# Optimization experiments

Measured on AMD Instinct MI355X. Metric: run time of the kernel, lower is better.

## Reference

```python
import jax, jax.numpy as jnp
import numpy as np

C = 256
RED = 8
DQK = C // RED  # 32


def setup_inputs() -> dict:
    key = jax.random.key(0)
    ks = jax.random.split(key, 8)
    B, H, W = 8, 64, 64
    x = jax.random.normal(ks[0], (B, C, H, W), dtype=jnp.float32)
    # 1x1 conv weights stored as [out, in]; biases [out]
    Wq = jax.random.normal(ks[1], (DQK, C), dtype=jnp.float32) * 0.02
    bq = jax.random.normal(ks[2], (DQK,), dtype=jnp.float32) * 0.02
    Wk = jax.random.normal(ks[3], (DQK, C), dtype=jnp.float32) * 0.02
    bk = jax.random.normal(ks[4], (DQK,), dtype=jnp.float32) * 0.02
    Wv = jax.random.normal(ks[5], (C, C), dtype=jnp.float32) * 0.02
    bv = jax.random.normal(ks[6], (C,), dtype=jnp.float32) * 0.02
    gamma = jax.random.normal(ks[7], (1,), dtype=jnp.float32) * 0.1
    return {"x": x, "Wq": Wq, "bq": bq, "Wk": Wk, "bk": bk, "Wv": Wv, "bv": bv, "gamma": gamma}


def reference(x, Wq, bq, Wk, bk, Wv, bv, gamma):
    B, Cc, H, W = x.shape
    N = H * W
    xf = x.reshape(B, Cc, N)                       # (B, C, N)
    # 1x1 convs == per-pixel dense projections
    q = jnp.einsum('dc,bcn->bdn', Wq, xf) + bq[None, :, None]   # (B, d, N)
    k = jnp.einsum('dc,bcn->bdn', Wk, xf) + bk[None, :, None]   # (B, d, N)
    v = jnp.einsum('ec,bcn->ben', Wv, xf) + bv[None, :, None]   # (B, C, N)
    # energy[b,i,j] = q[b,:,i] . k[b,:,j]; softmax over j (no scaling, SAGAN-style)
    energy = jnp.einsum('bdi,bdj->bij', q, k)      # (B, N, N)
    attn = jax.nn.softmax(energy, axis=-1)
    # out[b,c,i] = sum_j v[b,c,j] * attn[b,i,j]
    out = jnp.einsum('bcj,bij->bci', v, attn)      # (B, C, N)
    out = out.reshape(B, Cc, H, W)
    return gamma[0] * out + x
```

## Files before the change

kernel.cpp:

```cpp
#include <hip/hip_runtime.h>

#define NB 8
#define CCH 256
#define DQK 32
#define NPIX 4096

typedef __attribute__((ext_vector_type(8))) short short8;
typedef __attribute__((ext_vector_type(4))) float f32x4;
typedef __attribute__((ext_vector_type(4))) unsigned short ushort4v;

static __device__ __forceinline__ unsigned short f2bf(float f) {
  unsigned int u = __builtin_bit_cast(unsigned int, f);
  u += 0x7FFFu + ((u >> 16) & 1u);
  return (unsigned short)(u >> 16);
}
static __device__ __forceinline__ unsigned int pack2bf(float a, float b) {
  return (unsigned int)f2bf(a) | ((unsigned int)f2bf(b) << 16);
}

__global__ __launch_bounds__(256) void wconv_kernel(
    const float* __restrict__ Wq, const float* __restrict__ Wk,
    const float* __restrict__ Wv, unsigned short* __restrict__ Wbf) {
  const int e = (blockIdx.x * 256 + threadIdx.x) * 4;
  const int m = e >> 8, c = e & 255;
  const float* src;
  if (m < 32) src = Wq + (size_t)m * CCH;
  else if (m < 64) src = Wk + (size_t)(m - 32) * CCH;
  else src = Wv + (size_t)(m - 64) * CCH;
  const float4 v = *(const float4*)(src + c);
  ushort4v o;
  o[0] = f2bf(v.x); o[1] = f2bf(v.y); o[2] = f2bf(v.z); o[3] = f2bf(v.w);
  *(ushort4v*)(Wbf + e) = o;
}

__global__ __launch_bounds__(256) void proj_kernel(
    const float* __restrict__ x, const unsigned short* __restrict__ Wbf,
    const float* __restrict__ bq, const float* __restrict__ bk,
    const float* __restrict__ bv,
    unsigned short* __restrict__ Qb, unsigned short* __restrict__ Kb,
    unsigned short* __restrict__ Vb) {
  __shared__ unsigned short xs[32 * 256];
  const int t = threadIdx.x;
  const int b = blockIdx.x & 7;
  const int i0 = (blockIdx.x >> 3) * 32;
  const float* xb = x + (size_t)b * CCH * NPIX + i0;
  {
    const int ii = (t & 7) * 4;
    const int cb = t >> 3;
    const int sw8 = ((ii >> 2) & 7) << 3;
#pragma unroll
    for (int rep = 0; rep < 8; ++rep) {
      const int c = cb + 32 * rep;
      const float4 v = *(const float4*)(xb + (size_t)c * NPIX + ii);
      const float vv[4] = {v.x, v.y, v.z, v.w};
#pragma unroll
      for (int d = 0; d < 4; ++d) {
        const int cc = (c ^ sw8) ^ ((d & 1) << 4);
        xs[(ii + d) * 256 + cc] = f2bf(vv[d]);
      }
    }
  }
  __syncthreads();
  const int w = t >> 6, l = t & 63;
  const int lc = l & 15, lg = l >> 4;
  const int m0w = 80 * w;
  f32x4 acc[5][2];
#pragma unroll
  for (int mt = 0; mt < 5; ++mt)
#pragma unroll
    for (int nt = 0; nt < 2; ++nt) acc[mt][nt] = (f32x4){0.f, 0.f, 0.f, 0.f};

#pragma unroll
  for (int kk = 0; kk < 8; ++kk) {
    short8 af[5];
#pragma unroll
    for (int mt = 0; mt < 5; ++mt)
      af[mt] = *(const short8*)(Wbf + (size_t)(m0w + mt * 16 + lc) * CCH + kk * 32 + lg * 8);
#pragma unroll
    for (int nt = 0; nt < 2; ++nt) {
      const int i = nt * 16 + lc;
      const int s = (4 * nt + (lc >> 2)) & 7;
      const int cc = ((kk * 32 + lg * 8) ^ (s << 3)) ^ ((lc & 1) << 4);
      const short8 bfv = *(const short8*)&xs[i * 256 + cc];
#pragma unroll
      for (int mt = 0; mt < 5; ++mt)
        acc[mt][nt] = __builtin_amdgcn_mfma_f32_16x16x32_bf16(af[mt], bfv, acc[mt][nt], 0, 0, 0);
    }
  }
#pragma unroll
  for (int mt = 0; mt < 5; ++mt) {
    const int mbase = m0w + mt * 16;
    const int mrow = mbase + 4 * lg;
    if (mbase < 64) {
      const float* bias = (mbase < 32) ? (bq + mrow) : (bk + (mrow - 32));
      unsigned short* dst = (mbase < 32) ? (Qb + (size_t)b * NPIX * DQK + mrow)
                                         : (Kb + (size_t)b * NPIX * DQK + (mrow - 32));
      const float b0 = bias[0], b1 = bias[1], b2 = bias[2], b3 = bias[3];
#pragma unroll
      for (int nt = 0; nt < 2; ++nt) {
        const int i = i0 + nt * 16 + lc;
        ushort4v o;
        o[0] = f2bf(acc[mt][nt][0] + b0);
        o[1] = f2bf(acc[mt][nt][1] + b1);
        o[2] = f2bf(acc[mt][nt][2] + b2);
        o[3] = f2bf(acc[mt][nt][3] + b3);
        *(ushort4v*)(dst + (size_t)i * DQK) = o;
      }
    } else {
      const int vrow = mbase - 64 + 4 * lg;
#pragma unroll
      for (int jj = 0; jj < 4; ++jj) {
        const float bias = bv[vrow + jj];
        unsigned short* vdst = Vb + ((size_t)b * CCH + vrow + jj) * NPIX + i0;
#pragma unroll
        for (int nt = 0; nt < 2; ++nt)
          vdst[nt * 16 + lc] = f2bf(acc[mt][nt][jj] + bias);
      }
    }
  }
}

union AttnSmem {
  unsigned short p[2][64 * 64];
  float tsc[4][16 * 68];
};

__global__ __launch_bounds__(256, 2) void attn_kernel(
    const unsigned short* __restrict__ Qb,
    const unsigned short* __restrict__ Kb,
    const unsigned short* __restrict__ Vb,
    const float* __restrict__ x,
    const float* __restrict__ gammap,
    float* __restrict__ out) {
  __shared__ AttnSmem sm;
  __shared__ float l_lds[64];
  const int t = threadIdx.x;
  const int w = t >> 6, l = t & 63;
  const int lc = l & 15, lg = l >> 4;
  const int b = blockIdx.x & 7;
  const int q0 = (blockIdx.x >> 3) * 64;

  const unsigned short* Kl = Kb + (size_t)b * NPIX * DQK + (size_t)lc * DQK + lg * 8;
  const unsigned short* Vl = Vb + ((size_t)b * CCH + 64 * w + lc) * NPIX + lg * 8;
  const short8 qa = *(const short8*)(Qb + (size_t)b * NPIX * DQK +
                                     (size_t)(q0 + 16 * w + lc) * DQK + lg * 8);
  const f32x4 zero4 = {0.f, 0.f, 0.f, 0.f};
  const int pwb = (16 * w + lc) * 128;
  const int psw = (lc & 7) << 3;

  f32x4 acc[4][4];
#pragma unroll
  for (int mt = 0; mt < 4; ++mt)
#pragma unroll
    for (int ct = 0; ct < 4; ++ct) acc[mt][ct] = (f32x4){0.f, 0.f, 0.f, 0.f};
  float psum = 0.f;

  short8 vfA[8], vfB[8], kfA[4], kfB[4];

#pragma unroll
  for (int kt = 0; kt < 4; ++kt)
    kfA[kt] = *(const short8*)(Kl + (size_t)(kt * 16) * DQK);
#pragma unroll
  for (int kt = 0; kt < 4; ++kt) {
    const f32x4 s = __builtin_amdgcn_mfma_f32_16x16x32_bf16(kfA[kt], qa, zero4, 0, 0, 0);
    const float p0 = __expf(s[0]), p1 = __expf(s[1]);
    const float p2 = __expf(s[2]), p3 = __expf(s[3]);
    psum += (p0 + p1) + (p2 + p3);
    uint2 wv; wv.x = pack2bf(p0, p1); wv.y = pack2bf(p2, p3);
    *(uint2*)((char*)sm.p[0] + pwb + (((16 * kt + 4 * lg) ^ psw) << 1)) = wv;
  }
#pragma unroll
  for (int ct = 0; ct < 4; ++ct) {
    vfA[ct] = *(const short8*)(Vl + (size_t)(16 * ct) * NPIX);
    vfA[4 + ct] = *(const short8*)(Vl + (size_t)(16 * ct) * NPIX + 32);
  }
#pragma unroll
  for (int kt = 0; kt < 4; ++kt)
    kfB[kt] = *(const short8*)(Kl + (size_t)(64 + kt * 16) * DQK);
  __syncthreads();

#define ATTN_ITER(T, BUF, VF, KF_CUR, VF_NXT, KF_NXT)                               \
  {                                                                                 \
    const int t_ = (T);                                                             \
    if (t_ < 63) {                                                                  \
      const size_t kb2 = (size_t)(t_ + 1) * 64;                                     \
      _Pragma("unroll") for (int ct = 0; ct < 4; ++ct) {                            \
        VF_NXT[ct] = *(const short8*)(Vl + (size_t)(16 * ct) * NPIX + kb2);         \
        VF_NXT[4 + ct] = *(const short8*)(Vl + (size_t)(16 * ct) * NPIX + kb2 + 32);\
      }                                                                             \
      if (t_ < 62) {                                                                \
        const size_t kk2 = (size_t)(t_ + 2) * 64;                                   \
        _Pragma("unroll") for (int kt = 0; kt < 4; ++kt)                            \
          KF_NXT[kt] = *(const short8*)(Kl + (kk2 + kt * 16) * DQK);                \
      }                                                                             \
    }                                                                               \
    unsigned short* pb_ = sm.p[BUF];                                                \
    unsigned short* pb2_ = sm.p[(BUF) ^ 1];                                         \
    _Pragma("unroll") for (int ks2 = 0; ks2 < 2; ++ks2) {                           \
      short8 pa[4];                                                                 \
      _Pragma("unroll") for (int mt = 0; mt < 4; ++mt)                              \
        pa[mt] = *(const short8*)((const char*)pb_ + (16 * mt + lc) * 128 +         \
                                  (((32 * ks2 + 8 * lg) ^ psw) << 1));              \
      _Pragma("unroll") for (int ct = 0; ct < 4; ++ct)                              \
        _Pragma("unroll") for (int mt = 0; mt < 4; ++mt)                            \
          acc[mt][ct] = __builtin_amdgcn_mfma_f32_16x16x32_bf16(                    \
              pa[mt], VF[ks2 * 4 + ct], acc[mt][ct], 0, 0, 0);                      \
    }                                                                               \
    if (t_ < 63) {                                                                  \
      _Pragma("unroll") for (int kt = 0; kt < 4; ++kt) {                            \
        const f32x4 s = __builtin_amdgcn_mfma_f32_16x16x32_bf16(                    \
            KF_CUR[kt], qa, zero4, 0, 0, 0);                                        \
        const float p0 = __expf(s[0]), p1 = __expf(s[1]);                           \
        const float p2 = __expf(s[2]), p3 = __expf(s[3]);                           \
        psum += (p0 + p1) + (p2 + p3);                                              \
        uint2 wv; wv.x = pack2bf(p0, p1); wv.y = pack2bf(p2, p3);                   \
        *(uint2*)((char*)pb2_ + pwb + (((16 * kt + 4 * lg) ^ psw) << 1)) = wv;      \
      }                                                                             \
    }                                                                               \
    __syncthreads();                                                                \
  }

  for (int ks = 0; ks < 64; ks += 2) {
    ATTN_ITER(ks, 0, vfA, kfB, vfB, kfA);
    ATTN_ITER(ks + 1, 1, vfB, kfA, vfA, kfB);
  }
#undef ATTN_ITER

  {
    float v = psum;
    v += __shfl_xor(v, 16);
    v += __shfl_xor(v, 32);
    if (l < 16) l_lds[16 * w + lc] = v;
  }
  __syncthreads();

  const float g = gammap[0];
  float linv4[4][4];
#pragma unroll
  for (int mt = 0; mt < 4; ++mt)
#pragma unroll
    for (int jj = 0; jj < 4; ++jj)
      linv4[mt][jj] = 1.0f / l_lds[16 * mt + 4 * lg + jj];

  float* tw = sm.tsc[w];
  const float* xbp = x + (size_t)b * CCH * NPIX;
  float* ob = out + (size_t)b * CCH * NPIX;
#pragma unroll
  for (int ct = 0; ct < 4; ++ct) {
#pragma unroll
    for (int mt = 0; mt < 4; ++mt) {
      f32x4 o;
#pragma unroll
      for (int jj = 0; jj < 4; ++jj) o[jj] = g * acc[mt][ct][jj] * linv4[mt][jj];
      *(f32x4*)(tw + lc * 68 + 16 * mt + 4 * lg) = o;
    }
#pragma unroll
    for (int r = 0; r < 4; ++r) {
      const int crow = 4 * r + lg;
      const f32x4 o = *(const f32x4*)(tw + crow * 68 + lc * 4);
      const size_t idx = (size_t)(64 * w + 16 * ct + crow) * NPIX + (size_t)(q0 + lc * 4);
      const float4 xv = *(const float4*)(xbp + idx);
      float4 ov;
      ov.x = o[0] + xv.x; ov.y = o[1] + xv.y; ov.z = o[2] + xv.z; ov.w = o[3] + xv.w;
      *(float4*)(ob + idx) = ov;
    }
  }
}

extern "C" void kernel_launch(void* const* d_in, const int* in_sizes, int n_in,
                              void* d_out, int out_size, void* d_ws, size_t ws_size,
                              hipStream_t stream) {
  (void)in_sizes; (void)n_in; (void)out_size; (void)ws_size;
  const float* x     = (const float*)d_in[0];
  const float* Wq    = (const float*)d_in[1];
  const float* bq    = (const float*)d_in[2];
  const float* Wk    = (const float*)d_in[3];
  const float* bk    = (const float*)d_in[4];
  const float* Wv    = (const float*)d_in[5];
  const float* bv    = (const float*)d_in[6];
  const float* gamma = (const float*)d_in[7];

  unsigned short* Wbf = (unsigned short*)d_ws;
  unsigned short* Qb  = Wbf + 320 * CCH;
  unsigned short* Kb  = Qb + (size_t)NB * NPIX * DQK;
  unsigned short* Vb  = Kb + (size_t)NB * NPIX * DQK;

  wconv_kernel<<<80, 256, 0, stream>>>(Wq, Wk, Wv, Wbf);
  proj_kernel<<<1024, 256, 0, stream>>>(x, Wbf, bq, bk, bv, Qb, Kb, Vb);
  attn_kernel<<<512, 256, 0, stream>>>(Qb, Kb, Vb, x, gamma, (float*)d_out);
}
```

Before: 272.9 us.

## Use exp2 with prescaled Q, packed bf16 convert, and reschedule attention MFMAs

Q is now prescaled by log2(e) in the projection kernel, so the attention kernel can call exp2 directly instead of expf. The manual bf16 rounding is replaced by the hardware v_cvt_pk_bf16_f32 instruction. The QK score MFMAs are issued before the PV MFMAs so their latency overlaps. Both P fragment halves are loaded up front and the PV block runs under raised s_setprio. __syncthreads is replaced by an explicit lgkmcnt wait plus s_barrier, and gamma is folded into the reciprocal of the row sum. Rounding in the packed convert may differ slightly from the manual version, and holding extra fragments live raises register pressure.

```diff
diff --git a/kernel.cpp b/kernel.cpp
--- a/kernel.cpp
+++ b/kernel.cpp
@@ -14,8 +14,10 @@
   u += 0x7FFFu + ((u >> 16) & 1u);
   return (unsigned short)(u >> 16);
 }
-static __device__ __forceinline__ unsigned int pack2bf(float a, float b) {
-  return (unsigned int)f2bf(a) | ((unsigned int)f2bf(b) << 16);
+static __device__ __forceinline__ unsigned int cvt_pk_bf16(float a, float b) {
+  unsigned int r;
+  asm("v_cvt_pk_bf16_f32 %0, %1, %2" : "=v"(r) : "v"(a), "v"(b));
+  return r;
 }
 
 __global__ __launch_bounds__(256) void wconv_kernel(
@@ -92,18 +94,20 @@
     const int mbase = m0w + mt * 16;
     const int mrow = mbase + 4 * lg;
     if (mbase < 64) {
-      const float* bias = (mbase < 32) ? (bq + mrow) : (bk + (mrow - 32));
-      unsigned short* dst = (mbase < 32) ? (Qb + (size_t)b * NPIX * DQK + mrow)
-                                         : (Kb + (size_t)b * NPIX * DQK + (mrow - 32));
+      const bool isQ = (mbase < 32);
+      const float scale = isQ ? 1.44269504f : 1.0f;
+      const float* bias = isQ ? (bq + mrow) : (bk + (mrow - 32));
+      unsigned short* dst = isQ ? (Qb + (size_t)b * NPIX * DQK + mrow)
+                                : (Kb + (size_t)b * NPIX * DQK + (mrow - 32));
       const float b0 = bias[0], b1 = bias[1], b2 = bias[2], b3 = bias[3];
 #pragma unroll
       for (int nt = 0; nt < 2; ++nt) {
         const int i = i0 + nt * 16 + lc;
         ushort4v o;
-        o[0] = f2bf(acc[mt][nt][0] + b0);
-        o[1] = f2bf(acc[mt][nt][1] + b1);
-        o[2] = f2bf(acc[mt][nt][2] + b2);
-        o[3] = f2bf(acc[mt][nt][3] + b3);
+        o[0] = f2bf((acc[mt][nt][0] + b0) * scale);
+        o[1] = f2bf((acc[mt][nt][1] + b1) * scale);
+        o[2] = f2bf((acc[mt][nt][2] + b2) * scale);
+        o[3] = f2bf((acc[mt][nt][3] + b3) * scale);
         *(ushort4v*)(dst + (size_t)i * DQK) = o;
       }
     } else {
@@ -163,10 +167,10 @@
 #pragma unroll
   for (int kt = 0; kt < 4; ++kt) {
     const f32x4 s = __builtin_amdgcn_mfma_f32_16x16x32_bf16(kfA[kt], qa, zero4, 0, 0, 0);
-    const float p0 = __expf(s[0]), p1 = __expf(s[1]);
-    const float p2 = __expf(s[2]), p3 = __expf(s[3]);
+    const float p0 = __builtin_exp2f(s[0]), p1 = __builtin_exp2f(s[1]);
+    const float p2 = __builtin_exp2f(s[2]), p3 = __builtin_exp2f(s[3]);
     psum += (p0 + p1) + (p2 + p3);
-    uint2 wv; wv.x = pack2bf(p0, p1); wv.y = pack2bf(p2, p3);
+    uint2 wv; wv.x = cvt_pk_bf16(p0, p1); wv.y = cvt_pk_bf16(p2, p3);
     *(uint2*)((char*)sm.p[0] + pwb + (((16 * kt + 4 * lg) ^ psw) << 1)) = wv;
   }
 #pragma unroll
@@ -182,7 +186,7 @@
 #define ATTN_ITER(T, BUF, VF, KF_CUR, VF_NXT, KF_NXT)                               \
   {                                                                                 \
     const int t_ = (T);                                                             \
-    if (t_ < 63) {                                                                  \
+    if (t_ < 63) {           \
       const size_t kb2 = (size_t)(t_ + 1) * 64;                                     \
       _Pragma("unroll") for (int ct = 0; ct < 4; ++ct) {                            \
         VF_NXT[ct] = *(const short8*)(Vl + (size_t)(16 * ct) * NPIX + kb2);         \
@@ -194,30 +198,42 @@
           KF_NXT[kt] = *(const short8*)(Kl + (kk2 + kt * 16) * DQK);                \
       }                                                                             \
     }                                                                               \
+    f32x4 s_[4];                   \
+    if (t_ < 63) {                                                                  \
+      _Pragma("unroll") for (int kt = 0; kt < 4; ++kt)                              \
+        s_[kt] = __builtin_amdgcn_mfma_f32_16x16x32_bf16(KF_CUR[kt], qa, zero4, 0, 0, 0); \
+    }                                                                               \
     unsigned short* pb_ = sm.p[BUF];                                                \
     unsigned short* pb2_ = sm.p[(BUF) ^ 1];                                         \
-    _Pragma("unroll") for (int ks2 = 0; ks2 < 2; ++ks2) {                           \
-      short8 pa[4];                                                                 \
+    short8 pa0[4], pa1[4];                                                          \
+    _Pragma("unroll") for (int mt = 0; mt < 4; ++mt)                                \
+      pa0[mt] = *(const short8*)((const char*)pb_ + (16 * mt + lc) * 128 +          \
+                                 (((8 * lg) ^ psw) << 1));                          \
+    _Pragma("unroll") for (int mt = 0; mt < 4; ++mt)                                \
+      pa1[mt] = *(const short8*)((const char*)pb_ + (16 * mt + lc) * 128 +          \
+                                 (((32 + 8 * lg) ^ psw) << 1));                     \
+    __builtin_amdgcn_s_setprio(1);                                                  \
+    _Pragma("unroll") for (int ct = 0; ct < 4; ++ct)                                \
       _Pragma("unroll") for (int mt = 0; mt < 4; ++mt)                              \
-        pa[mt] = *(const short8*)((const char*)pb_ + (16 * mt + lc) * 128 +         \
-                                  (((32 * ks2 + 8 * lg) ^ psw) << 1));              \
-      _Pragma("unroll") for (int ct = 0; ct < 4; ++ct)                              \
-        _Pragma("unroll") for (int mt = 0; mt < 4; ++mt)                            \
-          acc[mt][ct] = __builtin_amdgcn_mfma_f32_16x16x32_bf16(                    \
-              pa[mt], VF[ks2 * 4 + ct], acc[mt][ct], 0, 0, 0);                      \
-    }                                                                               \
+        acc[mt][ct] = __builtin_amdgcn_mfma_f32_16x16x32_bf16(                      \
+            pa0[mt], VF[ct], acc[mt][ct], 0, 0, 0);                                 \
+    _Pragma("unroll") for (int ct = 0; ct < 4; ++ct)                                \
+      _Pragma("unroll") for (int mt = 0; mt < 4; ++mt)                              \
+        acc[mt][ct] = __builtin_amdgcn_mfma_f32_16x16x32_bf16(                      \
+            pa1[mt], VF[4 + ct], acc[mt][ct], 0, 0, 0);                             \
+    __builtin_amdgcn_s_setprio(0);                                                  \
     if (t_ < 63) {                                                                  \
       _Pragma("unroll") for (int kt = 0; kt < 4; ++kt) {                            \
-        const f32x4 s = __builtin_amdgcn_mfma_f32_16x16x32_bf16(                    \
-            KF_CUR[kt], qa, zero4, 0, 0, 0);                                        \
-        const float p0 = __expf(s[0]), p1 = __expf(s[1]);                           \
-        const float p2 = __expf(s[2]), p3 = __expf(s[3]);                           \
+        const float p0 = __builtin_exp2f(s_[kt][0]);                                \
+        const float p1 = __builtin_exp2f(s_[kt][1]);                                \
+        const float p2 = __builtin_exp2f(s_[kt][2]);                                \
+        const float p3 = __builtin_exp2f(s_[kt][3]);                                \
         psum += (p0 + p1) + (p2 + p3);                                              \
-        uint2 wv; wv.x = pack2bf(p0, p1); wv.y = pack2bf(p2, p3);                   \
+        uint2 wv; wv.x = cvt_pk_bf16(p0, p1); wv.y = cvt_pk_bf16(p2, p3);           \
         *(uint2*)((char*)pb2_ + pwb + (((16 * kt + 4 * lg) ^ psw) << 1)) = wv;      \
       }                                                                             \
     }                                                                               \
-    __syncthreads();                                                                \
+    asm volatile("s_waitcnt lgkmcnt(0)\n\ts_barrier" ::: "memory");                 \
   }
 
   for (int ks = 0; ks < 64; ks += 2) {
@@ -240,7 +256,7 @@
   for (int mt = 0; mt < 4; ++mt)
 #pragma unroll
     for (int jj = 0; jj < 4; ++jj)
-      linv4[mt][jj] = 1.0f / l_lds[16 * mt + 4 * lg + jj];
+      linv4[mt][jj] = g / l_lds[16 * mt + 4 * lg + jj];
 
   float* tw = sm.tsc[w];
   const float* xbp = x + (size_t)b * CCH * NPIX;
@@ -251,7 +267,7 @@
     for (int mt = 0; mt < 4; ++mt) {
       f32x4 o;
 #pragma unroll
-      for (int jj = 0; jj < 4; ++jj) o[jj] = g * acc[mt][ct][jj] * linv4[mt][jj];
+      for (int jj = 0; jj < 4; ++jj) o[jj] = acc[mt][ct][jj] * linv4[mt][jj];
       *(f32x4*)(tw + lc * 68 + 16 * mt + 4 * lg) = o;
     }
 #pragma unroll
```

After: 341.7 us. 25.2% more time.
